# Kernel tuning notes

Measured on AMD Instinct MI355X. Metric: run time of the kernel, lower is better.

Reference implementation:

```python
import jax, jax.numpy as jnp
import numpy as np

EMBED_DIM = 256
NUM_HEADS = 4
HEAD_DIM = EMBED_DIM // NUM_HEADS
SCALE = HEAD_DIM ** (-0.5)


def setup_inputs() -> dict:
    key = jax.random.key(0)
    kx, kq, kp, kb = jax.random.split(key, 4)
    B, N, C = 4, 4096, EMBED_DIM
    x = jax.random.normal(kx, (B, N, C), dtype=jnp.float32)
    # qkv: Linear(C, 3C, bias=False); torch stores weight as [out, in]
    w_qkv = jax.random.normal(kq, (3 * C, C), dtype=jnp.float32) * (C ** -0.5)
    w_proj = jax.random.normal(kp, (C, C), dtype=jnp.float32) * (C ** -0.5)
    b_proj = jax.random.normal(kb, (C,), dtype=jnp.float32) * 0.01
    return {"x": x, "w_qkv": w_qkv, "w_proj": w_proj, "b_proj": b_proj}


def reference(x, w_qkv, w_proj, b_proj):
    B, N, C = x.shape
    H, D = NUM_HEADS, HEAD_DIM
    # qkv projection: [B,N,3C] -> [3,B,H,N,D]
    qkv = (x @ w_qkv.T).reshape(B, N, 3, H, D).transpose(2, 0, 3, 1, 4)
    q, k, v = qkv[0], qkv[1], qkv[2]
    # materialized [B,H,N,N] scores (faithful to the original)
    attn = jnp.einsum("bhnd,bhmd->bhnm", q, k) * SCALE
    attn_probs = jax.nn.softmax(attn, axis=-1)
    out = jnp.einsum("bhnm,bhmd->bhnd", attn_probs, v)
    out = out.transpose(0, 2, 1, 3).reshape(B, N, C)
    return out @ w_proj.T + b_proj
```

## Files before the change

### kernel.cpp

```cpp
#include <hip/hip_runtime.h>
#include <hip/hip_bf16.h>

typedef __hip_bfloat16 bf16;
typedef _Float16 f16;
typedef __attribute__((ext_vector_type(8))) short bf16x8;
typedef __attribute__((ext_vector_type(8))) _Float16 f16x8;
typedef __attribute__((ext_vector_type(2))) _Float16 f16x2;
typedef __attribute__((ext_vector_type(4))) float f32x4;
typedef __attribute__((ext_vector_type(4))) unsigned int u32x4;
typedef __attribute__((ext_vector_type(2))) unsigned int u32x2;

#define B_ 4
#define N_ 4096
#define C_ 256
#define H_ 4
#define D_ 64
#define KLN 0.18033688011112042f

#if __has_builtin(__builtin_amdgcn_exp2f)
#define EXP2(x) __builtin_amdgcn_exp2f(x)
#else
#define EXP2(x) exp2f(x)
#endif
#if __has_builtin(__builtin_amdgcn_rcpf)
#define RCP(x) __builtin_amdgcn_rcpf(x)
#else
#define RCP(x) (1.0f / (x))
#endif

__device__ inline void load_lds16(const void* g, void* l) {
#if __has_builtin(__builtin_amdgcn_global_load_lds)
    __builtin_amdgcn_global_load_lds(
        (const __attribute__((address_space(1))) unsigned int*)g,
        (__attribute__((address_space(3))) unsigned int*)l, 16, 0, 0);
#else
    int ln = __lane_id();
    ((u32x4*)l)[ln] = *((const u32x4*)g);
#endif
}

__device__ inline unsigned int pk2(float a, float b) {
    unsigned int ua = __builtin_bit_cast(unsigned int, a) + 0x8000u;
    unsigned int ub = __builtin_bit_cast(unsigned int, b) + 0x8000u;
    return (ua >> 16) | (ub & 0xffff0000u);
}
__device__ inline unsigned int pkh2(float a, float b) {
#if __has_builtin(__builtin_amdgcn_cvt_pkrtz)
    return __builtin_bit_cast(unsigned int, __builtin_amdgcn_cvt_pkrtz(a, b));
#else
    f16x2 h = { (f16)a, (f16)b };
    return __builtin_bit_cast(unsigned int, h);
#endif
}

__global__ __launch_bounds__(256) void cast_bf16(const float* __restrict__ x,
                                                 const float* __restrict__ wq,
                                                 const float* __restrict__ wp,
                                                 bf16* __restrict__ xb,
                                                 bf16* __restrict__ wqb,
                                                 bf16* __restrict__ wpb)
{
    int bid = blockIdx.x;
    const float* s; bf16* d; int base;
    if (bid < 2048)      { s = x;  d = xb;  base = bid * 2048; }
    else if (bid < 2144) { s = wq; d = wqb; base = (bid - 2048) * 2048; }
    else                 { s = wp; d = wpb; base = (bid - 2144) * 2048; }
    int i = base + threadIdx.x * 8;
    f32x4 a = *reinterpret_cast<const f32x4*>(s + i);
    f32x4 b = *reinterpret_cast<const f32x4*>(s + i + 4);
    u32x4 o;
    o.x = pk2(a[0], a[1]); o.y = pk2(a[2], a[3]);
    o.z = pk2(b[0], b[1]); o.w = pk2(b[2], b[3]);
    *reinterpret_cast<u32x4*>(d + i) = o;
}

__global__ __launch_bounds__(256, 2) void qkv_fast(const bf16* __restrict__ x,
                                                   const bf16* __restrict__ w,
                                                   bf16* __restrict__ qw,
                                                   bf16* __restrict__ kw,
                                                   f16* __restrict__ vtw)
{
    __shared__ short w_s[64][264];
    const int tid  = threadIdx.x;
    const int lane = tid & 63;
    const int wav  = tid >> 6;
    const int quad = lane >> 4;
    const int l16  = lane & 15;
    const int bid = (blockIdx.x & 7) * 192 + (blockIdx.x >> 3);
    const int mt = bid / 12, nb = bid % 12;
    const int m0 = mt * 128, n0 = nb * 64;

    {
        const int row = tid >> 2, cb = (tid & 3) * 64;
        const bf16* src = w + (size_t)(n0 + row) * C_ + cb;
#pragma unroll
        for (int i = 0; i < 8; ++i)
            *reinterpret_cast<bf16x8*>(&w_s[row][cb + i * 8]) =
                *reinterpret_cast<const bf16x8*>(src + i * 8);
    }
    __syncthreads();

#pragma unroll
    for (int half = 0; half < 2; ++half) {
        const int mh = m0 + half * 64;
        f32x4 acc[4] = {{0,0,0,0},{0,0,0,0},{0,0,0,0},{0,0,0,0}};
        const bf16* xrow = x + (size_t)(mh + wav * 16 + l16) * C_ + quad * 8;
        if (nb < 8) {
#pragma unroll
            for (int k0 = 0; k0 < C_; k0 += 32) {
                bf16x8 a = *reinterpret_cast<const bf16x8*>(xrow + k0);
#pragma unroll
                for (int nt = 0; nt < 4; ++nt) {
                    bf16x8 b = *reinterpret_cast<const bf16x8*>(&w_s[nt * 16 + l16][k0 + quad * 8]);
                    acc[nt] = __builtin_amdgcn_mfma_f32_16x16x32_bf16(b, a, acc[nt], 0, 0, 0);
                }
            }
        } else {
#pragma unroll
            for (int k0 = 0; k0 < C_; k0 += 32) {
                bf16x8 a = *reinterpret_cast<const bf16x8*>(xrow + k0);
#pragma unroll
                for (int nt = 0; nt < 4; ++nt) {
                    bf16x8 b = *reinterpret_cast<const bf16x8*>(&w_s[nt * 16 + l16][k0 + quad * 8]);
                    acc[nt] = __builtin_amdgcn_mfma_f32_16x16x32_bf16(a, b, acc[nt], 0, 0, 0);
                }
            }
        }

        const int bb = mh >> 12;
        const int nbase = (mh + wav * 16) & (N_ - 1);
        if (nb < 4) {
            bf16* dst = qw + (((size_t)bb * H_ + nb) * N_ + nbase + l16) * D_;
#pragma unroll
            for (int nt = 0; nt < 4; ++nt) {
                u32x2 wv = { pk2(acc[nt][0] * KLN, acc[nt][1] * KLN),
                             pk2(acc[nt][2] * KLN, acc[nt][3] * KLN) };
                *reinterpret_cast<u32x2*>(dst + nt * 16 + quad * 4) = wv;
            }
        } else if (nb < 8) {
            bf16* dst = kw + (((size_t)bb * H_ + (nb - 4)) * N_ + nbase + l16) * D_;
#pragma unroll
            for (int nt = 0; nt < 4; ++nt) {
                u32x2 wv = { pk2(acc[nt][0], acc[nt][1]),
                             pk2(acc[nt][2], acc[nt][3]) };
                *reinterpret_cast<u32x2*>(dst + nt * 16 + quad * 4) = wv;
            }
        } else {
            const int h = nb - 8;
#pragma unroll
            for (int nt = 0; nt < 4; ++nt) {
                int d = nt * 16 + l16;
                u32x2 wv;
                wv.x = pkh2(acc[nt][0], acc[nt][1]);
                wv.y = pkh2(acc[nt][2], acc[nt][3]);
                *reinterpret_cast<u32x2*>(
                    vtw + (((size_t)bb * H_ + h) * D_ + d) * N_ + nbase + quad * 4) = wv;
            }
        }
    }
}

__global__ __launch_bounds__(512)
__attribute__((amdgpu_waves_per_eu(4, 4)))
void attn(const bf16* __restrict__ q,
          const bf16* __restrict__ k,
          const f16* __restrict__ vt,
          bf16* __restrict__ o)
{
    __shared__ __align__(16) char smem[81920];
    short* k_s = reinterpret_cast<short*>(smem);
    f16*   v_s = reinterpret_cast<f16*>(smem + 32768);

    const int tid  = threadIdx.x;
    const int lane = tid & 63;
    const int wav  = tid >> 6;
    const int quad = lane >> 4;
    const int l16  = lane & 15;
    const int l8   = lane & 7;
    const int sub  = wav & 3;
    const int jh   = wav >> 2;

    const int wg = (blockIdx.x & 7) * 64 + (blockIdx.x >> 3);
    const int bh = wg >> 5;
    const int qt = wg & 31;
    const int bb = bh >> 2, h = bh & 3;

    const bf16* qp = q  + (size_t)bh * N_ * D_;
    const bf16* kp = k  + (size_t)bh * N_ * D_;
    const f16*  vp = vt + (size_t)bh * D_ * N_;

    const int qbase = qt * 128 + sub * 32;
    bf16x8 qb[2][2];
#pragma unroll
    for (int qg = 0; qg < 2; ++qg)
#pragma unroll
        for (int ks = 0; ks < 2; ++ks)
            qb[qg][ks] = *reinterpret_cast<const bf16x8*>(
                qp + (size_t)(qbase + qg * 16 + l16) * D_ + ks * 32 + quad * 8);

    const int ri = lane >> 3;
    const int ci = lane & 7;
    const int gc = ci ^ ri;
    int koff[2], voff[2], lds_r[2];
#pragma unroll
    for (int g = 0; g < 2; ++g) {
        const int rb  = sub * 16 + g * 8;
        const int rho = rb + ri;
        const int pr  = (rho & 32) | ((rho & 12) << 1) | ((rho & 16) >> 2) | (rho & 3);
        koff[g]  = pr * D_ + gc * 8;
        voff[g]  = rho * N_ + gc * 8;
        lds_r[g] = rb * 64;
    }

    f32x4 oacc[2][4];
    f32x4 lacc[2];
#pragma unroll
    for (int qg = 0; qg < 2; ++qg) {
        lacc[qg] = (f32x4){0, 0, 0, 0};
#pragma unroll
        for (int dt = 0; dt < 4; ++dt) oacc[qg][dt] = (f32x4){0, 0, 0, 0};
    }
    const f16x8 onesA = {1.f16, 1.f16, 1.f16, 1.f16, 1.f16, 1.f16, 1.f16, 1.f16};

    f32x4 s[2][4];
    f16x8 pbE[2][2], pbO[2][2];

#define STAGE(kbuf, vslot, t) do {                                            \
    const int j0_ = jh * 2048 + (t) * 64;                                     \
    short* kd_ = k_s + ((kbuf) * 2 + jh) * 4096;                              \
    f16*   vd_ = v_s + ((vslot) * 2 + jh) * 4096;                             \
    load_lds16(kp + (size_t)j0_ * D_ + koff[0], kd_ + lds_r[0]);              \
    load_lds16(kp + (size_t)j0_ * D_ + koff[1], kd_ + lds_r[1]);              \
    load_lds16(vp + j0_ + voff[0],              vd_ + lds_r[0]);              \
    load_lds16(vp + j0_ + voff[1],              vd_ + lds_r[1]);              \
} while (0)

#define QK(kbuf) do {                                                         \
    const short* kt_ = k_s + ((kbuf) * 2 + jh) * 4096;                        \
    _Pragma("unroll")                                                         \
    for (int nt = 0; nt < 4; ++nt) {                                          \
        const int rb_ = (nt * 16 + l16) * 64;                                 \
        bf16x8 ka0_ = *reinterpret_cast<const bf16x8*>(kt_ + rb_ + ((quad    ) ^ l8) * 8); \
        bf16x8 ka1_ = *reinterpret_cast<const bf16x8*>(kt_ + rb_ + ((4 + quad) ^ l8) * 8); \
        _Pragma("unroll")                                                     \
        for (int qg = 0; qg < 2; ++qg) {                                      \
            s[qg][nt] = __builtin_amdgcn_mfma_f32_16x16x32_bf16(              \
                ka0_, qb[qg][0], (f32x4){0.f, 0.f, 0.f, 0.f}, 0, 0, 0);       \
            s[qg][nt] = __builtin_amdgcn_mfma_f32_16x16x32_bf16(              \
                ka1_, qb[qg][1], s[qg][nt], 0, 0, 0);                         \
        }                                                                     \
    }                                                                         \
} while (0)

#define PV(vslot, PB) do {                                                    \
    const f16* vt_ = v_s + ((vslot) * 2 + jh) * 4096;                         \
    lacc[0] = __builtin_amdgcn_mfma_f32_16x16x32_f16(onesA, PB[0][0], lacc[0], 0, 0, 0); \
    lacc[0] = __builtin_amdgcn_mfma_f32_16x16x32_f16(onesA, PB[0][1], lacc[0], 0, 0, 0); \
    lacc[1] = __builtin_amdgcn_mfma_f32_16x16x32_f16(onesA, PB[1][0], lacc[1], 0, 0, 0); \
    lacc[1] = __builtin_amdgcn_mfma_f32_16x16x32_f16(onesA, PB[1][1], lacc[1], 0, 0, 0); \
    _Pragma("unroll")                                                         \
    for (int ks = 0; ks < 2; ++ks) {                                          \
        _Pragma("unroll")                                                     \
        for (int dt = 0; dt < 4; ++dt) {                                      \
            f16x8 va_ = *reinterpret_cast<const f16x8*>(                      \
                vt_ + (dt * 16 + l16) * 64 + (((ks << 2) + quad) ^ l8) * 8);  \
            oacc[0][dt] = __builtin_amdgcn_mfma_f32_16x16x32_f16(va_, PB[0][ks], oacc[0][dt], 0, 0, 0); \
            oacc[1][dt] = __builtin_amdgcn_mfma_f32_16x16x32_f16(va_, PB[1][ks], oacc[1][dt], 0, 0, 0); \
        }                                                                     \
    }                                                                         \
} while (0)

#define EXPP(PB) do {                                                         \
    _Pragma("unroll")                                                         \
    for (int qg = 0; qg < 2; ++qg) {                                          \
        _Pragma("unroll")                                                     \
        for (int ks = 0; ks < 2; ++ks) {                                      \
            const f32x4 sa_ = s[qg][2 * ks], sb_ = s[qg][2 * ks + 1];         \
            u32x4 pw_;                                                        \
            pw_.x = pkh2(EXP2(sa_[0]), EXP2(sa_[1]));                         \
            pw_.y = pkh2(EXP2(sa_[2]), EXP2(sa_[3]));                         \
            pw_.z = pkh2(EXP2(sb_[0]), EXP2(sb_[1]));                         \
            pw_.w = pkh2(EXP2(sb_[2]), EXP2(sb_[3]));                         \
            PB[qg][ks] = __builtin_bit_cast(f16x8, pw_);                      \
        }                                                                     \
    }                                                                         \
} while (0)

#define SB __builtin_amdgcn_sched_barrier(0)

    STAGE(0, 0, 0);
    __syncthreads();

    STAGE(1, 1, 1);
    QK(0); EXPP(pbE);
    __syncthreads();

    STAGE(0, 2, 2);
    PV(0, pbE); SB; QK(1); EXPP(pbO);
    __syncthreads();

#pragma unroll 1
    for (int tb = 2; tb < 32; tb += 6) {
        STAGE(1, 0, tb + 1);
        PV(1, pbO); SB; QK(0); EXPP(pbE);
        __syncthreads();
        STAGE(0, 1, tb + 2);
        PV(2, pbE); SB; QK(1); EXPP(pbO);
        __syncthreads();
        STAGE(1, 2, tb + 3);
        PV(0, pbO); SB; QK(0); EXPP(pbE);
        __syncthreads();
        STAGE(0, 0, tb + 4);
        PV(1, pbE); SB; QK(1); EXPP(pbO);
        __syncthreads();
        STAGE(1, 1, tb + 5);
        PV(2, pbO); SB; QK(0); EXPP(pbE);
        __syncthreads();
        if (tb + 6 < 32) STAGE(0, 2, tb + 6);
        PV(0, pbE); SB; QK(1); EXPP(pbO);
        __syncthreads();
    }
    PV(1, pbO);

    __syncthreads();
    float* mrg = reinterpret_cast<float*>(smem);
    const int slot = (sub * 64 + lane) * 35;
    if (jh == 1) {
#pragma unroll
        for (int qg = 0; qg < 2; ++qg) {
#pragma unroll
            for (int dt = 0; dt < 4; ++dt)
#pragma unroll
                for (int e = 0; e < 4; ++e)
                    mrg[slot + qg * 17 + dt * 4 + e] = oacc[qg][dt][e];
            mrg[slot + qg * 17 + 16] = lacc[qg][0];
        }
    }
    __syncthreads();
    if (jh == 0) {
#pragma unroll
        for (int qg = 0; qg < 2; ++qg) {
            const float rl = RCP(lacc[qg][0] + mrg[slot + qg * 17 + 16]);
            const size_t obase = ((size_t)bb * N_ + qbase + qg * 16 + l16) * C_ + h * D_;
#pragma unroll
            for (int dt = 0; dt < 4; ++dt) {
                float v0 = (oacc[qg][dt][0] + mrg[slot + qg * 17 + dt * 4 + 0]) * rl;
                float v1 = (oacc[qg][dt][1] + mrg[slot + qg * 17 + dt * 4 + 1]) * rl;
                float v2 = (oacc[qg][dt][2] + mrg[slot + qg * 17 + dt * 4 + 2]) * rl;
                float v3 = (oacc[qg][dt][3] + mrg[slot + qg * 17 + dt * 4 + 3]) * rl;
                u32x2 wv = { pk2(v0, v1), pk2(v2, v3) };
                *reinterpret_cast<u32x2*>(o + obase + dt * 16 + quad * 4) = wv;
            }
        }
    }
}

__global__ __launch_bounds__(256, 2) void out_proj_fast(const bf16* __restrict__ ov,
                                                        const bf16* __restrict__ w,
                                                        const float* __restrict__ bias,
                                                        float* __restrict__ out)
{
    __shared__ short w_s[64][264];
    const int tid  = threadIdx.x;
    const int lane = tid & 63;
    const int wav  = tid >> 6;
    const int quad = lane >> 4;
    const int l16  = lane & 15;
    const int bid = (blockIdx.x & 7) * 64 + (blockIdx.x >> 3);
    const int m0 = (bid >> 2) * 128;
    const int n0 = (bid & 3) * 64;

    {
        const int row = tid >> 2, cb = (tid & 3) * 64;
        const bf16* src = w + (size_t)(n0 + row) * C_ + cb;
#pragma unroll
        for (int i = 0; i < 8; ++i)
            *reinterpret_cast<bf16x8*>(&w_s[row][cb + i * 8]) =
                *reinterpret_cast<const bf16x8*>(src + i * 8);
    }
    __syncthreads();

#pragma unroll
    for (int half = 0; half < 2; ++half) {
        const int mh = m0 + half * 64;
        f32x4 acc[4] = {{0,0,0,0},{0,0,0,0},{0,0,0,0},{0,0,0,0}};
        const bf16* orow = ov + (size_t)(mh + wav * 16 + l16) * C_ + quad * 8;
#pragma unroll
        for (int k0 = 0; k0 < C_; k0 += 32) {
            bf16x8 a = *reinterpret_cast<const bf16x8*>(orow + k0);
#pragma unroll
            for (int nt = 0; nt < 4; ++nt) {
                bf16x8 b = *reinterpret_cast<const bf16x8*>(&w_s[nt * 16 + l16][k0 + quad * 8]);
                acc[nt] = __builtin_amdgcn_mfma_f32_16x16x32_bf16(b, a, acc[nt], 0, 0, 0);
            }
        }
        const int m = mh + wav * 16 + l16;
#pragma unroll
        for (int nt = 0; nt < 4; ++nt) {
            const int oc0 = n0 + nt * 16 + quad * 4;
            f32x4 bv = *reinterpret_cast<const f32x4*>(bias + oc0);
            f32x4 ovv = acc[nt] + bv;
            *reinterpret_cast<f32x4*>(out + (size_t)m * C_ + oc0) = ovv;
        }
    }
}

extern "C" void kernel_launch(void* const* d_in, const int* in_sizes, int n_in,
                              void* d_out, int out_size, void* d_ws, size_t ws_size,
                              hipStream_t stream) {
    const float* x      = (const float*)d_in[0];
    const float* w_qkv  = (const float*)d_in[1];
    const float* w_proj = (const float*)d_in[2];
    const float* b_proj = (const float*)d_in[3];
    float* out = (float*)d_out;

    const size_t qkv_elems = (size_t)B_ * H_ * N_ * D_;
    bf16* q_ws  = (bf16*)d_ws;
    bf16* k_ws  = q_ws  + qkv_elems;
    f16*  vt_ws = (f16*)(k_ws + qkv_elems);
    bf16* o_ws  = (bf16*)(vt_ws + qkv_elems);
    bf16* x_bf  = o_ws  + qkv_elems;
    bf16* wq_bf = x_bf  + (size_t)B_ * N_ * C_;
    bf16* wp_bf = wq_bf + (size_t)3 * C_ * C_;

    cast_bf16    <<<2176, 256, 0, stream>>>(x, w_qkv, w_proj, x_bf, wq_bf, wp_bf);
    qkv_fast     <<<1536, 256, 0, stream>>>(x_bf, wq_bf, q_ws, k_ws, vt_ws);
    attn         <<< 512, 512, 0, stream>>>(q_ws, k_ws, vt_ws, o_ws);
    out_proj_fast<<< 512, 256, 0, stream>>>(o_ws, wp_bf, b_proj, out);
}
```

Before: 186.1 us.

## Drop KV split in attention block; each wave processes full key range

The attention block previously used 8 waves, split into two halves that each covered half of the key sequence, followed by an LDS merge of partial outputs and row sums. Now a 256-thread block with 4 waves walks all 64 key tiles itself, using half the LDS, and the cross-half merge and its extra barriers are gone. The trade is fewer waves per block and a serial loop twice as long per wave. It also relies on two blocks per CU to keep enough waves resident to hide memory latency.

After: 174.3 us. 6.4% less time.

```diff
diff --git a/kernel.cpp b/kernel.cpp
--- a/kernel.cpp
+++ b/kernel.cpp
@@ -160,16 +160,14 @@
     }
 }
 
-__global__ __launch_bounds__(512)
-__attribute__((amdgpu_waves_per_eu(4, 4)))
-void attn(const bf16* __restrict__ q,
-          const bf16* __restrict__ k,
-          const f16* __restrict__ vt,
-          bf16* __restrict__ o)
+__global__ __launch_bounds__(256, 2) void attn(const bf16* __restrict__ q,
+                                               const bf16* __restrict__ k,
+                                               const f16* __restrict__ vt,
+                                               bf16* __restrict__ o)
 {
-    __shared__ __align__(16) char smem[81920];
+    __shared__ __align__(16) char smem[40960];
     short* k_s = reinterpret_cast<short*>(smem);
-    f16*   v_s = reinterpret_cast<f16*>(smem + 32768);
+    f16*   v_s = reinterpret_cast<f16*>(smem + 16384);
 
     const int tid  = threadIdx.x;
     const int lane = tid & 63;
@@ -177,8 +175,6 @@
     const int quad = lane >> 4;
     const int l16  = lane & 15;
     const int l8   = lane & 7;
-    const int sub  = wav & 3;
-    const int jh   = wav >> 2;
 
     const int wg = (blockIdx.x & 7) * 64 + (blockIdx.x >> 3);
     const int bh = wg >> 5;
@@ -189,7 +185,7 @@
     const bf16* kp = k  + (size_t)bh * N_ * D_;
     const f16*  vp = vt + (size_t)bh * D_ * N_;
 
-    const int qbase = qt * 128 + sub * 32;
+    const int qbase = qt * 128 + wav * 32;
     bf16x8 qb[2][2];
 #pragma unroll
     for (int qg = 0; qg < 2; ++qg)
@@ -204,7 +200,7 @@
     int koff[2], voff[2], lds_r[2];
 #pragma unroll
     for (int g = 0; g < 2; ++g) {
-        const int rb  = sub * 16 + g * 8;
+        const int rb  = wav * 16 + g * 8;
         const int rho = rb + ri;
         const int pr  = (rho & 32) | ((rho & 12) << 1) | ((rho & 16) >> 2) | (rho & 3);
         koff[g]  = pr * D_ + gc * 8;
@@ -226,9 +222,9 @@
     f16x8 pbE[2][2], pbO[2][2];
 
 #define STAGE(kbuf, vslot, t) do {                                            \
-    const int j0_ = jh * 2048 + (t) * 64;                                     \
-    short* kd_ = k_s + ((kbuf) * 2 + jh) * 4096;                              \
-    f16*   vd_ = v_s + ((vslot) * 2 + jh) * 4096;                             \
+    const int j0_ = (t) * 64;                                                 \
+    short* kd_ = k_s + (kbuf) * 4096;                                         \
+    f16*   vd_ = v_s + (vslot) * 4096;                                        \
     load_lds16(kp + (size_t)j0_ * D_ + koff[0], kd_ + lds_r[0]);              \
     load_lds16(kp + (size_t)j0_ * D_ + koff[1], kd_ + lds_r[1]);              \
     load_lds16(vp + j0_ + voff[0],              vd_ + lds_r[0]);              \
@@ -236,7 +232,7 @@
 } while (0)
 
 #define QK(kbuf) do {                                                         \
-    const short* kt_ = k_s + ((kbuf) * 2 + jh) * 4096;                        \
+    const short* kt_ = k_s + (kbuf) * 4096;                                   \
     _Pragma("unroll")                                                         \
     for (int nt = 0; nt < 4; ++nt) {                                          \
         const int rb_ = (nt * 16 + l16) * 64;                                 \
@@ -253,7 +249,7 @@
 } while (0)
 
 #define PV(vslot, PB) do {                                                    \
-    const f16* vt_ = v_s + ((vslot) * 2 + jh) * 4096;                         \
+    const f16* vt_ = v_s + (vslot) * 4096;                                    \
     lacc[0] = __builtin_amdgcn_mfma_f32_16x16x32_f16(onesA, PB[0][0], lacc[0], 0, 0, 0); \
     lacc[0] = __builtin_amdgcn_mfma_f32_16x16x32_f16(onesA, PB[0][1], lacc[0], 0, 0, 0); \
     lacc[1] = __builtin_amdgcn_mfma_f32_16x16x32_f16(onesA, PB[1][0], lacc[1], 0, 0, 0); \
@@ -300,7 +296,7 @@
     __syncthreads();
 
 #pragma unroll 1
-    for (int tb = 2; tb < 32; tb += 6) {
+    for (int tb = 2; tb <= 56; tb += 6) {
         STAGE(1, 0, tb + 1);
         PV(1, pbO); SB; QK(0); EXPP(pbE);
         __syncthreads();
@@ -316,41 +312,28 @@
         STAGE(1, 1, tb + 5);
         PV(2, pbO); SB; QK(0); EXPP(pbE);
         __syncthreads();
-        if (tb + 6 < 32) STAGE(0, 2, tb + 6);
+        STAGE(0, 2, tb + 6);
         PV(0, pbE); SB; QK(1); EXPP(pbO);
         __syncthreads();
     }
-    PV(1, pbO);
-
-    __syncthreads();
-    float* mrg = reinterpret_cast<float*>(smem);
-    const int slot = (sub * 64 + lane) * 35;
-    if (jh == 1) {
-#pragma unroll
-        for (int qg = 0; qg < 2; ++qg) {
-#pragma unroll
-            for (int dt = 0; dt < 4; ++dt)
-#pragma unroll
-                for (int e = 0; e < 4; ++e)
-                    mrg[slot + qg * 17 + dt * 4 + e] = oacc[qg][dt][e];
-            mrg[slot + qg * 17 + 16] = lacc[qg][0];
-        }
-    }
-    __syncthreads();
-    if (jh == 0) {
-#pragma unroll
-        for (int qg = 0; qg < 2; ++qg) {
-            const float rl = RCP(lacc[qg][0] + mrg[slot + qg * 17 + 16]);
-            const size_t obase = ((size_t)bb * N_ + qbase + qg * 16 + l16) * C_ + h * D_;
-#pragma unroll
-            for (int dt = 0; dt < 4; ++dt) {
-                float v0 = (oacc[qg][dt][0] + mrg[slot + qg * 17 + dt * 4 + 0]) * rl;
-                float v1 = (oacc[qg][dt][1] + mrg[slot + qg * 17 + dt * 4 + 1]) * rl;
-                float v2 = (oacc[qg][dt][2] + mrg[slot + qg * 17 + dt * 4 + 2]) * rl;
-                float v3 = (oacc[qg][dt][3] + mrg[slot + qg * 17 + dt * 4 + 3]) * rl;
-                u32x2 wv = { pk2(v0, v1), pk2(v2, v3) };
-                *reinterpret_cast<u32x2*>(o + obase + dt * 16 + quad * 4) = wv;
-            }
+    STAGE(1, 0, 63);
+    PV(1, pbO); SB; QK(0); EXPP(pbE);
+    __syncthreads();
+    PV(2, pbE); SB; QK(1); EXPP(pbO);
+    PV(0, pbO);
+
+#pragma unroll
+    for (int qg = 0; qg < 2; ++qg) {
+        const float rl = RCP(lacc[qg][0]);
+        const size_t obase = ((size_t)bb * N_ + qbase + qg * 16 + l16) * C_ + h * D_;
+#pragma unroll
+        for (int dt = 0; dt < 4; ++dt) {
+            float v0 = oacc[qg][dt][0] * rl;
+            float v1 = oacc[qg][dt][1] * rl;
+            float v2 = oacc[qg][dt][2] * rl;
+            float v3 = oacc[qg][dt][3] * rl;
+            u32x2 wv = { pk2(v0, v1), pk2(v2, v3) };
+            *reinterpret_cast<u32x2*>(o + obase + dt * 16 + quad * 4) = wv;
         }
     }
 }
@@ -425,6 +408,6 @@
 
     cast_bf16    <<<2176, 256, 0, stream>>>(x, w_qkv, w_proj, x_bf, wq_bf, wp_bf);
     qkv_fast     <<<1536, 256, 0, stream>>>(x_bf, wq_bf, q_ws, k_ws, vt_ws);
-    attn         <<< 512, 512, 0, stream>>>(q_ws, k_ws, vt_ws, o_ws);
+    attn         <<< 512, 256, 0, stream>>>(q_ws, k_ws, vt_ws, o_ws);
     out_proj_fast<<< 512, 256, 0, stream>>>(o_ws, wp_bf, b_proj, out);
 }
```
